# Kernel tuning notes

Measured on AMD Instinct MI355X. Metric: run time of the kernel, lower is better.

The kernel has to match this reference:

```python
import jax, jax.numpy as jnp
import numpy as np

D_MODEL = 768
NUM_HEADS = 8
HEAD_DIM = D_MODEL // NUM_HEADS


def setup_inputs() -> dict:
    key = jax.random.key(0)
    ks = jax.random.split(key, 5)
    B, N = 4, 2048
    scale = 1.0 / np.sqrt(D_MODEL)
    return {
        "x": jax.random.normal(ks[0], (B, N, D_MODEL), dtype=jnp.float32),
        "W_qkv": jax.random.normal(ks[1], (D_MODEL, 3 * D_MODEL), dtype=jnp.float32) * scale,
        "b_qkv": jax.random.normal(ks[2], (3 * D_MODEL,), dtype=jnp.float32) * 0.01,
        "W_out": jax.random.normal(ks[3], (D_MODEL, D_MODEL), dtype=jnp.float32) * scale,
        "b_out": jax.random.normal(ks[4], (D_MODEL,), dtype=jnp.float32) * 0.01,
    }


def reference(x, W_qkv, b_qkv, W_out, b_out):
    B, N, _ = x.shape
    H, Dh = NUM_HEADS, HEAD_DIM
    # fused QKV projection: [B,N,3*D] -> [3,B,H,N,Dh]
    qkv = (x @ W_qkv + b_qkv).reshape(B, N, 3, H, Dh).transpose(2, 0, 3, 1, 4)
    q, k, v = qkv[0], qkv[1], qkv[2]
    # full NxN attention, as in the original (no masking)
    scores = jnp.einsum("bhnd,bhmd->bhnm", q, k) / jnp.sqrt(jnp.float32(Dh)).astype(x.dtype)
    weights = jax.nn.softmax(scores, axis=-1)
    out = jnp.einsum("bhnm,bhmd->bhnd", weights, v)  # [B,H,N,Dh]
    out = out.transpose(0, 2, 1, 3).reshape(B, N, H * Dh)
    return out @ W_out + b_out
```

## Files before the change

### kernel.cpp

```cpp
#include <hip/hip_runtime.h>
#include <hip/hip_bf16.h>
#include <math.h>

#define BB      4
#define NN      2048
#define DM      768
#define NH      8
#define DHH     96
#define BH      (BB*NH)
#define MROWS   (BB*NN)
#define NC_QKV  (3*DM)

typedef short v4s  __attribute__((ext_vector_type(4)));
typedef short v8s  __attribute__((ext_vector_type(8)));
typedef float v4f  __attribute__((ext_vector_type(4)));
typedef float v16f __attribute__((ext_vector_type(16)));
typedef unsigned int u32;

#define SCQ 0.14724599350930152f

static __device__ __forceinline__ ushort f2bf(float f) {
    __hip_bfloat16 h = __float2bfloat16(f);
    return *reinterpret_cast<ushort*>(&h);
}

static __device__ __forceinline__ void gload_lds16(const ushort* g, ushort* l) {
    __builtin_amdgcn_global_load_lds(
        (const __attribute__((address_space(1))) void*)g,
        (__attribute__((address_space(3))) void*)l, 16, 0, 0);
}

static __device__ __forceinline__ v8s load2x4_o16(const ushort* p) {
    union { v4s h[2]; v8s s; } x;
    x.h[0] = *reinterpret_cast<const v4s*>(p);
    x.h[1] = *reinterpret_cast<const v4s*>(p + 16);
    return x.s;
}

static __device__ __forceinline__ v8s pack4(u32 a, u32 b, u32 c, u32 d) {
    union { u32 u[4]; v8s s; } x;
    x.u[0] = a; x.u[1] = b; x.u[2] = c; x.u[3] = d;
    return x.s;
}
static __device__ __forceinline__ u32 bfpair(float lo, float hi) {
    return (u32)f2bf(lo) | ((u32)f2bf(hi) << 16);
}

__global__ __launch_bounds__(256)
void conv_bf16(const float* __restrict__ in, ushort* __restrict__ out, int n8)
{
    int i = blockIdx.x * 256 + threadIdx.x;
    if (i >= n8) return;
    const float4* p = reinterpret_cast<const float4*>(in) + (size_t)i * 2;
    float4 a = p[0], b = p[1];
    ushort r[8] = {f2bf(a.x), f2bf(a.y), f2bf(a.z), f2bf(a.w),
                   f2bf(b.x), f2bf(b.y), f2bf(b.z), f2bf(b.w)};
    *reinterpret_cast<v8s*>(out + (size_t)i * 8) = *reinterpret_cast<v8s*>(r);
}

__global__ __launch_bounds__(256)
void convT_bf16(const float* __restrict__ W, ushort* __restrict__ Wt, int K, int N)
{
    __shared__ ushort t[32][33];
    const int k0 = blockIdx.x * 32, n0 = blockIdx.y * 32;
    const int tx = threadIdx.x & 31, ty = threadIdx.x >> 5;
    #pragma unroll
    for (int r = ty; r < 32; r += 8)
        t[tx][r] = f2bf(W[(size_t)(k0 + r) * N + n0 + tx]);
    __syncthreads();
    #pragma unroll
    for (int r = ty; r < 32; r += 8)
        Wt[(size_t)(n0 + r) * K + k0 + tx] = t[r][tx];
}

template<int SCATTER>
__global__ __launch_bounds__(256)
void gemm_mfma(const ushort* __restrict__ A, const ushort* __restrict__ Bt,
               const float* __restrict__ bias, void* __restrict__ outp,
               int K, int Ncols)
{
    __shared__ ushort As[2][8192];
    __shared__ ushort Bs[2][8192];

    const int tid  = threadIdx.x;
    const int lane = tid & 63;
    const int wv   = tid >> 6;
    const int l31  = lane & 31;
    const int lhi  = lane >> 5;
    const int wr   = wv >> 1, wc = wv & 1;

    const int ny   = gridDim.y;
    const int id   = blockIdx.y * gridDim.x + blockIdx.x;
    const int c8   = id & 7;
    const int j    = id >> 3;
    const int hy   = (j >= (ny >> 1) * 8) ? 1 : 0;
    const int w    = j - hy * (ny >> 1) * 8;
    const int bx   = c8 * 8 + (w & 7);
    const int by   = hy * (ny >> 1) + (w >> 3);
    const int row0 = bx * 128;
    const int col0 = by * 128;

    v16f acc[2][2];
    #pragma unroll
    for (int mi = 0; mi < 2; ++mi)
        #pragma unroll
        for (int nj = 0; nj < 2; ++nj)
            #pragma unroll
            for (int i = 0; i < 16; ++i) acc[mi][nj][i] = 0.0f;

#define STAGE_G(bsel, kk) do {                                                  \
    _Pragma("unroll")                                                           \
    for (int c = 0; c < 4; ++c) {                                               \
        const int g   = c * 4 + wv;                                             \
        const int idx = g * 64 + lane;                                          \
        const int ss  = idx >> 7, rr = idx & 127;                               \
        gload_lds16(&A [(size_t)(row0 + rr) * K + (kk) + ss * 8],               \
                    &As[bsel][g * 512]);                                        \
        gload_lds16(&Bt[(size_t)(col0 + rr) * K + (kk) + ss * 8],               \
                    &Bs[bsel][g * 512]);                                        \
    }                                                                           \
} while (0)

    STAGE_G(0, 0);
    __syncthreads();

    const int nk = K >> 6;
    for (int t = 0; t < nk; ++t) {
        const int cur = t & 1;
        if (t + 1 < nk) STAGE_G(cur ^ 1, (t + 1) << 6);

        #pragma unroll
        for (int s16 = 0; s16 < 4; ++s16) {
            const int ks = s16 * 2 + lhi;
            v8s a0 = *reinterpret_cast<const v8s*>(&As[cur][(size_t)(ks * 128 + 64 * wr + l31) * 8]);
            v8s a1 = *reinterpret_cast<const v8s*>(&As[cur][(size_t)(ks * 128 + 64 * wr + 32 + l31) * 8]);
            v8s b0 = *reinterpret_cast<const v8s*>(&Bs[cur][(size_t)(ks * 128 + 64 * wc + l31) * 8]);
            v8s b1 = *reinterpret_cast<const v8s*>(&Bs[cur][(size_t)(ks * 128 + 64 * wc + 32 + l31) * 8]);
            acc[0][0] = __builtin_amdgcn_mfma_f32_32x32x16_bf16(a0, b0, acc[0][0], 0, 0, 0);
            acc[0][1] = __builtin_amdgcn_mfma_f32_32x32x16_bf16(a0, b1, acc[0][1], 0, 0, 0);
            acc[1][0] = __builtin_amdgcn_mfma_f32_32x32x16_bf16(a1, b0, acc[1][0], 0, 0, 0);
            acc[1][1] = __builtin_amdgcn_mfma_f32_32x32x16_bf16(a1, b1, acc[1][1], 0, 0, 0);
        }
        __syncthreads();
    }
#undef STAGE_G

    #pragma unroll
    for (int nj = 0; nj < 2; ++nj) {
        const int c = col0 + 64 * wc + 32 * nj + l31;
        const float bv = bias[c];
        #pragma unroll
        for (int mi = 0; mi < 2; ++mi) {
            #pragma unroll
            for (int r = 0; r < 16; ++r) {
                const int m = row0 + 64 * wr + 32 * mi + (r & 3) + 8 * (r >> 2) + 4 * lhi;
                float v = acc[mi][nj][r] + bv;
                if (SCATTER) {
                    const int s   = c / DM;
                    const int rem = c - s * DM;
                    const int h   = rem / DHH;
                    const int d   = rem - h * DHH;
                    const int b   = m >> 11;
                    const int n   = m & (NN - 1);
                    if (s == 0) v *= SCQ;
                    ((ushort*)outp)[((size_t)(s * BH + b * NH + h) * NN + n) * DHH + d] = f2bf(v);
                } else {
                    ((float*)outp)[(size_t)m * Ncols + c] = v;
                }
            }
        }
    }
}

__global__ __launch_bounds__(256, 4)
void attn_mfma(const ushort* __restrict__ qkv, ushort* __restrict__ attnout)
{
    __shared__ ushort Ks[6144];
    __shared__ ushort Vt[96][68];

    const int tid  = threadIdx.x;
    const int lane = tid & 63;
    const int wv   = tid >> 6;
    const int l15  = lane & 15;
    const int g4   = lane >> 4;

    const int id   = blockIdx.y * gridDim.x + blockIdx.x;
    const int c8   = id & 7;
    const int j    = id >> 3;
    const int bh   = c8 * 4 + (j & 3);
    const int qt   = j >> 2;
    const int q0   = qt * 64;
    const int b    = bh >> 3, h = bh & 7;

    const ushort* Qg = qkv + (size_t)bh * NN * DHH;
    const ushort* Kg = qkv + ((size_t)BH + bh) * NN * DHH;
    const ushort* Vg = qkv + ((size_t)2 * BH + bh) * NN * DHH;

    const int qrow = q0 + wv * 16 + l15;
    v8s qf[3];
    #pragma unroll
    for (int c = 0; c < 3; ++c)
        qf[c] = *reinterpret_cast<const v8s*>(&Qg[(size_t)qrow * DHH + c * 32 + g4 * 8]);

    v4f o[6];
    #pragma unroll
    for (int dt = 0; dt < 6; ++dt)
        #pragma unroll
        for (int i = 0; i < 4; ++i) o[dt][i] = 0.0f;
    float ds = 0.0f;

    {
        const size_t rowb = (size_t)lane * DHH;
        v8s kr[3], vr[3];
        #pragma unroll
        for (int i = 0; i < 3; ++i) {
            kr[i] = *reinterpret_cast<const v8s*>(&Kg[rowb + (wv * 3 + i) * 8]);
            vr[i] = *reinterpret_cast<const v8s*>(&Vg[rowb + (i * 4 + wv) * 8]);
        }
        #pragma unroll
        for (int i = 0; i < 3; ++i) {
            *reinterpret_cast<v8s*>(&Ks[(wv * 3 + i) * 512 + lane * 8]) = kr[i];
            #pragma unroll
            for (int jj = 0; jj < 8; ++jj)
                Vt[(i * 4 + wv) * 8 + jj][lane] = (ushort)vr[i][jj];
        }
    }
    __syncthreads();

    for (int t = 0; t < 32; ++t) {
        v8s kr0, kr1, kr2, vr0, vr1, vr2;
        if (t < 31) {
            const size_t rowb = (size_t)((t + 1) * 64 + lane) * DHH;
            kr0 = *reinterpret_cast<const v8s*>(&Kg[rowb + (wv * 3 + 0) * 8]);
            kr1 = *reinterpret_cast<const v8s*>(&Kg[rowb + (wv * 3 + 1) * 8]);
            kr2 = *reinterpret_cast<const v8s*>(&Kg[rowb + (wv * 3 + 2) * 8]);
            vr0 = *reinterpret_cast<const v8s*>(&Vg[rowb + (0 * 4 + wv) * 8]);
            vr1 = *reinterpret_cast<const v8s*>(&Vg[rowb + (1 * 4 + wv) * 8]);
            vr2 = *reinterpret_cast<const v8s*>(&Vg[rowb + (2 * 4 + wv) * 8]);
        }

        #pragma unroll
        for (int th = 0; th < 2; ++th) {
            v4f s0, s1;
            #pragma unroll
            for (int i = 0; i < 4; ++i) { s0[i] = 0.0f; s1[i] = 0.0f; }
            __builtin_amdgcn_s_setprio(1);
            #pragma unroll
            for (int c = 0; c < 3; ++c) {
                v8s kf0 = *reinterpret_cast<const v8s*>(
                    &Ks[((c * 4 + g4) * 64 + (th * 2 + 0) * 16 + l15) * 8]);
                v8s kf1 = *reinterpret_cast<const v8s*>(
                    &Ks[((c * 4 + g4) * 64 + (th * 2 + 1) * 16 + l15) * 8]);
                s0 = __builtin_amdgcn_mfma_f32_16x16x32_bf16(kf0, qf[c], s0, 0, 0, 0);
                s1 = __builtin_amdgcn_mfma_f32_16x16x32_bf16(kf1, qf[c], s1, 0, 0, 0);
            }
            __builtin_amdgcn_s_setprio(0);

            float e0[4], e1[4];
            #pragma unroll
            for (int r = 0; r < 4; ++r) {
                e0[r] = exp2f(s0[r]);
                e1[r] = exp2f(s1[r]);
                ds += e0[r] + e1[r];
            }
            v8s pf = pack4(bfpair(e0[0], e0[1]), bfpair(e0[2], e0[3]),
                           bfpair(e1[0], e1[1]), bfpair(e1[2], e1[3]));

            __builtin_amdgcn_s_setprio(1);
            #pragma unroll
            for (int dt = 0; dt < 6; ++dt) {
                const ushort* vp = &Vt[dt * 16 + l15][th * 32 + g4 * 4];
                v8s va = load2x4_o16(vp);
                o[dt] = __builtin_amdgcn_mfma_f32_16x16x32_bf16(va, pf, o[dt], 0, 0, 0);
            }
            __builtin_amdgcn_s_setprio(0);
        }

        if (t < 31) {
            __syncthreads();
            *reinterpret_cast<v8s*>(&Ks[(wv * 3 + 0) * 512 + lane * 8]) = kr0;
            *reinterpret_cast<v8s*>(&Ks[(wv * 3 + 1) * 512 + lane * 8]) = kr1;
            *reinterpret_cast<v8s*>(&Ks[(wv * 3 + 2) * 512 + lane * 8]) = kr2;
            #pragma unroll
            for (int jj = 0; jj < 8; ++jj) Vt[(0 * 4 + wv) * 8 + jj][lane] = (ushort)vr0[jj];
            #pragma unroll
            for (int jj = 0; jj < 8; ++jj) Vt[(1 * 4 + wv) * 8 + jj][lane] = (ushort)vr1[jj];
            #pragma unroll
            for (int jj = 0; jj < 8; ++jj) Vt[(2 * 4 + wv) * 8 + jj][lane] = (ushort)vr2[jj];
            __syncthreads();
        }
    }

    ds += __shfl_xor(ds, 16, 64);
    ds += __shfl_xor(ds, 32, 64);
    const float inv = 1.0f / ds;

    const int n = q0 + wv * 16 + l15;
    ushort* orow = attnout + ((size_t)(b * NN + n)) * DM + h * DHH;
    #pragma unroll
    for (int dt = 0; dt < 6; ++dt) {
        const int d0 = dt * 16 + g4 * 4;
        uint2 pk;
        pk.x = bfpair(o[dt][0] * inv, o[dt][1] * inv);
        pk.y = bfpair(o[dt][2] * inv, o[dt][3] * inv);
        *reinterpret_cast<uint2*>(&orow[d0]) = pk;
    }
}

extern "C" void kernel_launch(void* const* d_in, const int* in_sizes, int n_in,
                              void* d_out, int out_size, void* d_ws, size_t ws_size,
                              hipStream_t stream)
{
    (void)in_sizes; (void)n_in; (void)out_size; (void)ws_size;
    const float* x    = (const float*)d_in[0];
    const float* Wqkv = (const float*)d_in[1];
    const float* bqkv = (const float*)d_in[2];
    const float* Wout = (const float*)d_in[3];
    const float* bout = (const float*)d_in[4];
    float* out = (float*)d_out;

    ushort* qkv   = (ushort*)d_ws;
    ushort* ao    = qkv   + (size_t)3 * BH * NN * DHH;
    ushort* xbf   = ao    + (size_t)MROWS * DM;
    ushort* wqkvt = xbf   + (size_t)MROWS * DM;
    ushort* woutt = wqkvt + (size_t)DM * NC_QKV;

    dim3 blk(256);

    conv_bf16<<<dim3(MROWS * DM / 8 / 256), blk, 0, stream>>>(x, xbf, MROWS * DM / 8);
    convT_bf16<<<dim3(DM / 32, NC_QKV / 32), blk, 0, stream>>>(Wqkv, wqkvt, DM, NC_QKV);
    convT_bf16<<<dim3(DM / 32, DM / 32), blk, 0, stream>>>(Wout, woutt, DM, DM);

    gemm_mfma<1><<<dim3(MROWS / 128, NC_QKV / 128), blk, 0, stream>>>(
        xbf, wqkvt, bqkv, (void*)qkv, DM, NC_QKV);

    attn_mfma<<<dim3(32, 32), blk, 0, stream>>>(qkv, ao);

    gemm_mfma<0><<<dim3(MROWS / 128, DM / 128), blk, 0, stream>>>(
        ao, woutt, bout, (void*)out, DM, DM);
}
```

Measured before the change: 209.2 us.

## Split KV tile across waves and reduce partial attention outputs in LDS

The attention kernel now has every wave handle all 64 query rows of the block against its own 32-key slice of a 128-key tile, instead of each wave owning 16 queries and sweeping all keys. This halves the number of K/V tile iterations and barriers and lets each V fragment load feed four MFMAs, cutting LDS reads per MFMA. The cost is a cross-wave reduction of the output accumulators and row sums through shared memory at the end, more registers (launch bounds drop to 2 blocks per SM), and a larger LDS footprint. V loading is also restructured so that threads pack pairs of rows into wide LDS stores for the transposed layout.

```diff
diff --git a/kernel.cpp b/kernel.cpp
--- a/kernel.cpp
+++ b/kernel.cpp
@@ -172,11 +172,13 @@
     }
 }
 
-__global__ __launch_bounds__(256, 4)
+#define VTB 12288
+#define DSB 6400
+
+__global__ __launch_bounds__(256, 2)
 void attn_mfma(const ushort* __restrict__ qkv, ushort* __restrict__ attnout)
 {
-    __shared__ ushort Ks[6144];
-    __shared__ ushort Vt[96][68];
+    __shared__ ushort smem[25344];
 
     const int tid  = threadIdx.x;
     const int lane = tid & 63;
@@ -188,122 +190,200 @@
     const int c8   = id & 7;
     const int j    = id >> 3;
     const int bh   = c8 * 4 + (j & 3);
-    const int qt   = j >> 2;
-    const int q0   = qt * 64;
+    const int qblk = j >> 2;
+    const int q0   = qblk * 64;
     const int b    = bh >> 3, h = bh & 7;
 
     const ushort* Qg = qkv + (size_t)bh * NN * DHH;
     const ushort* Kg = qkv + ((size_t)BH + bh) * NN * DHH;
     const ushort* Vg = qkv + ((size_t)2 * BH + bh) * NN * DHH;
 
-    const int qrow = q0 + wv * 16 + l15;
-    v8s qf[3];
-    #pragma unroll
-    for (int c = 0; c < 3; ++c)
-        qf[c] = *reinterpret_cast<const v8s*>(&Qg[(size_t)qrow * DHH + c * 32 + g4 * 8]);
-
-    v4f o[6];
+    v8s qf[4][3];
+    #pragma unroll
+    for (int qt = 0; qt < 4; ++qt)
+        #pragma unroll
+        for (int c = 0; c < 3; ++c)
+            qf[qt][c] = *reinterpret_cast<const v8s*>(
+                &Qg[(size_t)(q0 + qt * 16 + l15) * DHH + c * 32 + g4 * 8]);
+
+    v4f of[6][4];
     #pragma unroll
     for (int dt = 0; dt < 6; ++dt)
         #pragma unroll
-        for (int i = 0; i < 4; ++i) o[dt][i] = 0.0f;
-    float ds = 0.0f;
+        for (int qt = 0; qt < 4; ++qt)
+            #pragma unroll
+            for (int i = 0; i < 4; ++i) of[dt][qt][i] = 0.0f;
+    float ds4[4] = {0.0f, 0.0f, 0.0f, 0.0f};
+
+    int kgo[6], klo[6];
+    #pragma unroll
+    for (int i = 0; i < 6; ++i) {
+        const int u = i * 256 + tid;
+        const int r = u / 12, c = u - r * 12;
+        kgo[i] = r * DHH + c * 8;
+        klo[i] = (c * 128 + r) * 8;
+    }
+    const int  kvb = (tid & 15) * 8;
+    const int  dg  = tid >> 4;
+    const size_t vgo = (size_t)kvb * DHH + dg * 8;
+    const int  vlo = VTB + dg * 8 * 136 + kvb;
 
     {
-        const size_t rowb = (size_t)lane * DHH;
-        v8s kr[3], vr[3];
-        #pragma unroll
-        for (int i = 0; i < 3; ++i) {
-            kr[i] = *reinterpret_cast<const v8s*>(&Kg[rowb + (wv * 3 + i) * 8]);
-            vr[i] = *reinterpret_cast<const v8s*>(&Vg[rowb + (i * 4 + wv) * 8]);
-        }
-        #pragma unroll
-        for (int i = 0; i < 3; ++i) {
-            *reinterpret_cast<v8s*>(&Ks[(wv * 3 + i) * 512 + lane * 8]) = kr[i];
-            #pragma unroll
-            for (int jj = 0; jj < 8; ++jj)
-                Vt[(i * 4 + wv) * 8 + jj][lane] = (ushort)vr[i][jj];
+        v8s kr[6];
+        #pragma unroll
+        for (int i = 0; i < 6; ++i)
+            kr[i] = *reinterpret_cast<const v8s*>(&Kg[kgo[i]]);
+        v8s vr[8];
+        if (tid < 192) {
+            #pragma unroll
+            for (int r = 0; r < 8; ++r)
+                vr[r] = *reinterpret_cast<const v8s*>(&Vg[vgo + (size_t)r * DHH]);
+        }
+        #pragma unroll
+        for (int i = 0; i < 6; ++i)
+            *reinterpret_cast<v8s*>(&smem[klo[i]]) = kr[i];
+        if (tid < 192) {
+            #pragma unroll
+            for (int j8 = 0; j8 < 8; ++j8) {
+                u32 w0 = (u32)(ushort)vr[0][j8] | ((u32)(ushort)vr[1][j8] << 16);
+                u32 w1 = (u32)(ushort)vr[2][j8] | ((u32)(ushort)vr[3][j8] << 16);
+                u32 w2 = (u32)(ushort)vr[4][j8] | ((u32)(ushort)vr[5][j8] << 16);
+                u32 w3 = (u32)(ushort)vr[6][j8] | ((u32)(ushort)vr[7][j8] << 16);
+                *reinterpret_cast<v8s*>(&smem[vlo + j8 * 136]) = pack4(w0, w1, w2, w3);
+            }
         }
     }
     __syncthreads();
 
-    for (int t = 0; t < 32; ++t) {
-        v8s kr0, kr1, kr2, vr0, vr1, vr2;
-        if (t < 31) {
-            const size_t rowb = (size_t)((t + 1) * 64 + lane) * DHH;
-            kr0 = *reinterpret_cast<const v8s*>(&Kg[rowb + (wv * 3 + 0) * 8]);
-            kr1 = *reinterpret_cast<const v8s*>(&Kg[rowb + (wv * 3 + 1) * 8]);
-            kr2 = *reinterpret_cast<const v8s*>(&Kg[rowb + (wv * 3 + 2) * 8]);
-            vr0 = *reinterpret_cast<const v8s*>(&Vg[rowb + (0 * 4 + wv) * 8]);
-            vr1 = *reinterpret_cast<const v8s*>(&Vg[rowb + (1 * 4 + wv) * 8]);
-            vr2 = *reinterpret_cast<const v8s*>(&Vg[rowb + (2 * 4 + wv) * 8]);
-        }
-
-        #pragma unroll
-        for (int th = 0; th < 2; ++th) {
+    for (int t = 0; t < 16; ++t) {
+        const bool have = (t < 15);
+        const size_t tb = (size_t)(t + 1) * 128 * DHH;
+
+        v8s kr[6];
+        if (have) {
+            #pragma unroll
+            for (int i = 0; i < 6; ++i)
+                kr[i] = *reinterpret_cast<const v8s*>(&Kg[tb + kgo[i]]);
+        }
+
+        v8s pb[4];
+        #pragma unroll
+        for (int qt = 0; qt < 4; ++qt) {
             v4f s0, s1;
             #pragma unroll
             for (int i = 0; i < 4; ++i) { s0[i] = 0.0f; s1[i] = 0.0f; }
             __builtin_amdgcn_s_setprio(1);
             #pragma unroll
             for (int c = 0; c < 3; ++c) {
-                v8s kf0 = *reinterpret_cast<const v8s*>(
-                    &Ks[((c * 4 + g4) * 64 + (th * 2 + 0) * 16 + l15) * 8]);
-                v8s kf1 = *reinterpret_cast<const v8s*>(
-                    &Ks[((c * 4 + g4) * 64 + (th * 2 + 1) * 16 + l15) * 8]);
-                s0 = __builtin_amdgcn_mfma_f32_16x16x32_bf16(kf0, qf[c], s0, 0, 0, 0);
-                s1 = __builtin_amdgcn_mfma_f32_16x16x32_bf16(kf1, qf[c], s1, 0, 0, 0);
+                const int kb = ((c * 4 + g4) * 128 + wv * 32 + l15) * 8;
+                v8s kf0 = *reinterpret_cast<const v8s*>(&smem[kb]);
+                v8s kf1 = *reinterpret_cast<const v8s*>(&smem[kb + 128]);
+                s0 = __builtin_amdgcn_mfma_f32_16x16x32_bf16(kf0, qf[qt][c], s0, 0, 0, 0);
+                s1 = __builtin_amdgcn_mfma_f32_16x16x32_bf16(kf1, qf[qt][c], s1, 0, 0, 0);
             }
             __builtin_amdgcn_s_setprio(0);
-
-            float e0[4], e1[4];
-            #pragma unroll
-            for (int r = 0; r < 4; ++r) {
-                e0[r] = exp2f(s0[r]);
-                e1[r] = exp2f(s1[r]);
-                ds += e0[r] + e1[r];
-            }
-            v8s pf = pack4(bfpair(e0[0], e0[1]), bfpair(e0[2], e0[3]),
-                           bfpair(e1[0], e1[1]), bfpair(e1[2], e1[3]));
-
-            __builtin_amdgcn_s_setprio(1);
-            #pragma unroll
-            for (int dt = 0; dt < 6; ++dt) {
-                const ushort* vp = &Vt[dt * 16 + l15][th * 32 + g4 * 4];
-                v8s va = load2x4_o16(vp);
-                o[dt] = __builtin_amdgcn_mfma_f32_16x16x32_bf16(va, pf, o[dt], 0, 0, 0);
-            }
-            __builtin_amdgcn_s_setprio(0);
-        }
-
-        if (t < 31) {
+            float e00 = exp2f(s0[0]), e01 = exp2f(s0[1]),
+                  e02 = exp2f(s0[2]), e03 = exp2f(s0[3]);
+            float e10 = exp2f(s1[0]), e11 = exp2f(s1[1]),
+                  e12 = exp2f(s1[2]), e13 = exp2f(s1[3]);
+            ds4[qt] += ((e00 + e01) + (e02 + e03)) + ((e10 + e11) + (e12 + e13));
+            pb[qt] = pack4(bfpair(e00, e01), bfpair(e02, e03),
+                           bfpair(e10, e11), bfpair(e12, e13));
+        }
+
+        v8s vr[8];
+        if (have) {
             __syncthreads();
-            *reinterpret_cast<v8s*>(&Ks[(wv * 3 + 0) * 512 + lane * 8]) = kr0;
-            *reinterpret_cast<v8s*>(&Ks[(wv * 3 + 1) * 512 + lane * 8]) = kr1;
-            *reinterpret_cast<v8s*>(&Ks[(wv * 3 + 2) * 512 + lane * 8]) = kr2;
-            #pragma unroll
-            for (int jj = 0; jj < 8; ++jj) Vt[(0 * 4 + wv) * 8 + jj][lane] = (ushort)vr0[jj];
-            #pragma unroll
-            for (int jj = 0; jj < 8; ++jj) Vt[(1 * 4 + wv) * 8 + jj][lane] = (ushort)vr1[jj];
-            #pragma unroll
-            for (int jj = 0; jj < 8; ++jj) Vt[(2 * 4 + wv) * 8 + jj][lane] = (ushort)vr2[jj];
+            #pragma unroll
+            for (int i = 0; i < 6; ++i)
+                *reinterpret_cast<v8s*>(&smem[klo[i]]) = kr[i];
+            if (tid < 192) {
+                #pragma unroll
+                for (int r = 0; r < 8; ++r)
+                    vr[r] = *reinterpret_cast<const v8s*>(&Vg[tb + vgo + (size_t)r * DHH]);
+            }
+        }
+
+        __builtin_amdgcn_s_setprio(1);
+        #pragma unroll
+        for (int dt = 0; dt < 6; ++dt) {
+            const ushort* vp = &smem[VTB + (dt * 16 + l15) * 136 + wv * 32 + g4 * 4];
+            v8s va = load2x4_o16(vp);
+            #pragma unroll
+            for (int qt = 0; qt < 4; ++qt)
+                of[dt][qt] = __builtin_amdgcn_mfma_f32_16x16x32_bf16(va, pb[qt], of[dt][qt], 0, 0, 0);
+        }
+        __builtin_amdgcn_s_setprio(0);
+
+        if (have) {
             __syncthreads();
-        }
-    }
-
-    ds += __shfl_xor(ds, 16, 64);
-    ds += __shfl_xor(ds, 32, 64);
-    const float inv = 1.0f / ds;
-
-    const int n = q0 + wv * 16 + l15;
-    ushort* orow = attnout + ((size_t)(b * NN + n)) * DM + h * DHH;
-    #pragma unroll
-    for (int dt = 0; dt < 6; ++dt) {
-        const int d0 = dt * 16 + g4 * 4;
-        uint2 pk;
-        pk.x = bfpair(o[dt][0] * inv, o[dt][1] * inv);
-        pk.y = bfpair(o[dt][2] * inv, o[dt][3] * inv);
-        *reinterpret_cast<uint2*>(&orow[d0]) = pk;
+            if (tid < 192) {
+                #pragma unroll
+                for (int j8 = 0; j8 < 8; ++j8) {
+                    u32 w0 = (u32)(ushort)vr[0][j8] | ((u32)(ushort)vr[1][j8] << 16);
+                    u32 w1 = (u32)(ushort)vr[2][j8] | ((u32)(ushort)vr[3][j8] << 16);
+                    u32 w2 = (u32)(ushort)vr[4][j8] | ((u32)(ushort)vr[5][j8] << 16);
+                    u32 w3 = (u32)(ushort)vr[6][j8] | ((u32)(ushort)vr[7][j8] << 16);
+                    *reinterpret_cast<v8s*>(&smem[vlo + j8 * 136]) = pack4(w0, w1, w2, w3);
+                }
+            }
+            __syncthreads();
+        }
+    }
+
+    #pragma unroll
+    for (int qt = 0; qt < 4; ++qt) {
+        ds4[qt] += __shfl_xor(ds4[qt], 16, 64);
+        ds4[qt] += __shfl_xor(ds4[qt], 32, 64);
+    }
+    __syncthreads();
+    float* fsm = reinterpret_cast<float*>(smem);
+    if (lane < 16) {
+        #pragma unroll
+        for (int qt = 0; qt < 4; ++qt)
+            fsm[DSB + wv * 64 + qt * 16 + lane] = ds4[qt];
+    }
+    for (int w = 0; w < 3; ++w) {
+        if (wv == w) {
+            #pragma unroll
+            for (int dt = 0; dt < 6; ++dt)
+                #pragma unroll
+                for (int qt = 0; qt < 4; ++qt) {
+                    float* p = &fsm[(qt * 16 + l15) * 100 + dt * 16 + g4 * 4];
+                    if (w == 0) {
+                        *reinterpret_cast<v4f*>(p) = of[dt][qt];
+                    } else {
+                        v4f tmp = *reinterpret_cast<const v4f*>(p);
+                        tmp += of[dt][qt];
+                        *reinterpret_cast<v4f*>(p) = tmp;
+                    }
+                }
+        }
+        __syncthreads();
+    }
+    if (wv == 3) {
+        float inv[4];
+        #pragma unroll
+        for (int qt = 0; qt < 4; ++qt) {
+            const int q = qt * 16 + l15;
+            inv[qt] = 1.0f / (fsm[DSB + q] + fsm[DSB + 64 + q] +
+                              fsm[DSB + 128 + q] + fsm[DSB + 192 + q]);
+        }
+        #pragma unroll
+        for (int dt = 0; dt < 6; ++dt)
+            #pragma unroll
+            for (int qt = 0; qt < 4; ++qt) {
+                v4f tmp = *reinterpret_cast<const v4f*>(
+                    &fsm[(qt * 16 + l15) * 100 + dt * 16 + g4 * 4]);
+                tmp += of[dt][qt];
+                const float iv = inv[qt];
+                uint2 pk;
+                pk.x = bfpair(tmp[0] * iv, tmp[1] * iv);
+                pk.y = bfpair(tmp[2] * iv, tmp[3] * iv);
+                *reinterpret_cast<uint2*>(
+                    &attnout[((size_t)(b * NN + q0 + qt * 16 + l15)) * DM +
+                             h * DHH + dt * 16 + g4 * 4]) = pk;
+            }
     }
 }
 
```

Measured after the change: 270.0 us. +29.1%, slower.

## Process two query tiles per wave in attention to reuse K/V fragments

Applied to the files above, without the earlier changes.

Each attention block now handles 128 query rows instead of 64, with every wave computing two 16-row query tiles that share the same K and V fragments loaded from LDS. This halves the K/V global loads and LDS staging per query row, and halves the grid. The cost is roughly double the accumulator and Q registers per thread, with launch bounds relaxed to 2 blocks per CU. Only 512 blocks remain, which lowers occupancy and latency hiding.

```diff
diff --git a/kernel.cpp b/kernel.cpp
--- a/kernel.cpp
+++ b/kernel.cpp
@@ -172,7 +172,7 @@
     }
 }
 
-__global__ __launch_bounds__(256, 4)
+__global__ __launch_bounds__(256, 2)
 void attn_mfma(const ushort* __restrict__ qkv, ushort* __restrict__ attnout)
 {
     __shared__ ushort Ks[6144];
@@ -188,26 +188,30 @@
     const int c8   = id & 7;
     const int j    = id >> 3;
     const int bh   = c8 * 4 + (j & 3);
-    const int qt   = j >> 2;
-    const int q0   = qt * 64;
+    const int qblk = j >> 2;
+    const int q0   = qblk * 128;
     const int b    = bh >> 3, h = bh & 7;
 
     const ushort* Qg = qkv + (size_t)bh * NN * DHH;
     const ushort* Kg = qkv + ((size_t)BH + bh) * NN * DHH;
     const ushort* Vg = qkv + ((size_t)2 * BH + bh) * NN * DHH;
 
-    const int qrow = q0 + wv * 16 + l15;
-    v8s qf[3];
-    #pragma unroll
-    for (int c = 0; c < 3; ++c)
-        qf[c] = *reinterpret_cast<const v8s*>(&Qg[(size_t)qrow * DHH + c * 32 + g4 * 8]);
-
-    v4f o[6];
-    #pragma unroll
-    for (int dt = 0; dt < 6; ++dt)
-        #pragma unroll
-        for (int i = 0; i < 4; ++i) o[dt][i] = 0.0f;
-    float ds = 0.0f;
+    v8s qf[2][3];
+    #pragma unroll
+    for (int qt = 0; qt < 2; ++qt)
+        #pragma unroll
+        for (int c = 0; c < 3; ++c)
+            qf[qt][c] = *reinterpret_cast<const v8s*>(
+                &Qg[(size_t)(q0 + wv * 32 + qt * 16 + l15) * DHH + c * 32 + g4 * 8]);
+
+    v4f o[2][6];
+    #pragma unroll
+    for (int qt = 0; qt < 2; ++qt)
+        #pragma unroll
+        for (int dt = 0; dt < 6; ++dt)
+            #pragma unroll
+            for (int i = 0; i < 4; ++i) o[qt][dt][i] = 0.0f;
+    float ds[2] = {0.0f, 0.0f};
 
     {
         const size_t rowb = (size_t)lane * DHH;
@@ -241,9 +245,11 @@
 
         #pragma unroll
         for (int th = 0; th < 2; ++th) {
-            v4f s0, s1;
-            #pragma unroll
-            for (int i = 0; i < 4; ++i) { s0[i] = 0.0f; s1[i] = 0.0f; }
+            v4f s00, s01, s10, s11;
+            #pragma unroll
+            for (int i = 0; i < 4; ++i) {
+                s00[i] = 0.0f; s01[i] = 0.0f; s10[i] = 0.0f; s11[i] = 0.0f;
+            }
             __builtin_amdgcn_s_setprio(1);
             #pragma unroll
             for (int c = 0; c < 3; ++c) {
@@ -251,27 +257,36 @@
                     &Ks[((c * 4 + g4) * 64 + (th * 2 + 0) * 16 + l15) * 8]);
                 v8s kf1 = *reinterpret_cast<const v8s*>(
                     &Ks[((c * 4 + g4) * 64 + (th * 2 + 1) * 16 + l15) * 8]);
-                s0 = __builtin_amdgcn_mfma_f32_16x16x32_bf16(kf0, qf[c], s0, 0, 0, 0);
-                s1 = __builtin_amdgcn_mfma_f32_16x16x32_bf16(kf1, qf[c], s1, 0, 0, 0);
+                s00 = __builtin_amdgcn_mfma_f32_16x16x32_bf16(kf0, qf[0][c], s00, 0, 0, 0);
+                s01 = __builtin_amdgcn_mfma_f32_16x16x32_bf16(kf1, qf[0][c], s01, 0, 0, 0);
+                s10 = __builtin_amdgcn_mfma_f32_16x16x32_bf16(kf0, qf[1][c], s10, 0, 0, 0);
+                s11 = __builtin_amdgcn_mfma_f32_16x16x32_bf16(kf1, qf[1][c], s11, 0, 0, 0);
             }
             __builtin_amdgcn_s_setprio(0);
 
-            float e0[4], e1[4];
-            #pragma unroll
-            for (int r = 0; r < 4; ++r) {
-                e0[r] = exp2f(s0[r]);
-                e1[r] = exp2f(s1[r]);
-                ds += e0[r] + e1[r];
-            }
-            v8s pf = pack4(bfpair(e0[0], e0[1]), bfpair(e0[2], e0[3]),
-                           bfpair(e1[0], e1[1]), bfpair(e1[2], e1[3]));
+            v8s pf[2];
+            #pragma unroll
+            for (int qt = 0; qt < 2; ++qt) {
+                const v4f& sa = qt ? s10 : s00;
+                const v4f& sb = qt ? s11 : s01;
+                float e0[4], e1[4];
+                #pragma unroll
+                for (int r = 0; r < 4; ++r) {
+                    e0[r] = exp2f(sa[r]);
+                    e1[r] = exp2f(sb[r]);
+                    ds[qt] += e0[r] + e1[r];
+                }
+                pf[qt] = pack4(bfpair(e0[0], e0[1]), bfpair(e0[2], e0[3]),
+                               bfpair(e1[0], e1[1]), bfpair(e1[2], e1[3]));
+            }
 
             __builtin_amdgcn_s_setprio(1);
             #pragma unroll
             for (int dt = 0; dt < 6; ++dt) {
                 const ushort* vp = &Vt[dt * 16 + l15][th * 32 + g4 * 4];
                 v8s va = load2x4_o16(vp);
-                o[dt] = __builtin_amdgcn_mfma_f32_16x16x32_bf16(va, pf, o[dt], 0, 0, 0);
+                o[0][dt] = __builtin_amdgcn_mfma_f32_16x16x32_bf16(va, pf[0], o[0][dt], 0, 0, 0);
+                o[1][dt] = __builtin_amdgcn_mfma_f32_16x16x32_bf16(va, pf[1], o[1][dt], 0, 0, 0);
             }
             __builtin_amdgcn_s_setprio(0);
         }
@@ -291,19 +306,22 @@
         }
     }
 
-    ds += __shfl_xor(ds, 16, 64);
-    ds += __shfl_xor(ds, 32, 64);
-    const float inv = 1.0f / ds;
-
-    const int n = q0 + wv * 16 + l15;
-    ushort* orow = attnout + ((size_t)(b * NN + n)) * DM + h * DHH;
-    #pragma unroll
-    for (int dt = 0; dt < 6; ++dt) {
-        const int d0 = dt * 16 + g4 * 4;
-        uint2 pk;
-        pk.x = bfpair(o[dt][0] * inv, o[dt][1] * inv);
-        pk.y = bfpair(o[dt][2] * inv, o[dt][3] * inv);
-        *reinterpret_cast<uint2*>(&orow[d0]) = pk;
+    #pragma unroll
+    for (int qt = 0; qt < 2; ++qt) {
+        float d = ds[qt];
+        d += __shfl_xor(d, 16, 64);
+        d += __shfl_xor(d, 32, 64);
+        const float inv = 1.0f / d;
+        const int n = q0 + wv * 32 + qt * 16 + l15;
+        ushort* orow = attnout + ((size_t)(b * NN + n)) * DM + h * DHH;
+        #pragma unroll
+        for (int dt = 0; dt < 6; ++dt) {
+            const int d0 = dt * 16 + g4 * 4;
+            uint2 pk;
+            pk.x = bfpair(o[qt][dt][0] * inv, o[qt][dt][1] * inv);
+            pk.y = bfpair(o[qt][dt][2] * inv, o[qt][dt][3] * inv);
+            *reinterpret_cast<uint2*>(&orow[d0]) = pk;
+        }
     }
 }
 
@@ -334,7 +352,7 @@
     gemm_mfma<1><<<dim3(MROWS / 128, NC_QKV / 128), blk, 0, stream>>>(
         xbf, wqkvt, bqkv, (void*)qkv, DM, NC_QKV);
 
-    attn_mfma<<<dim3(32, 32), blk, 0, stream>>>(qkv, ao);
+    attn_mfma<<<dim3(16, 32), blk, 0, stream>>>(qkv, ao);
 
     gemm_mfma<0><<<dim3(MROWS / 128, DM / 128), blk, 0, stream>>>(
         ao, woutt, bout, (void*)out, DM, DM);
```

After: 204.5 us. 2.2% less time.
